# Performance work log

Measured on AMD Instinct MI355X. Metric: run time of the kernel, lower is better.

Reference implementation:

```python
import jax, jax.numpy as jnp
import numpy as np

B, N, D, H, COND = 1, 1024, 1024, 16, 128
S = 2 * N          # noisy tokens + clean x0 tokens
BS = 16            # diffusion block size
HD = D // H        # head dim = 64


def _ln(x, w):
    # LayerNorm module: F.layer_norm in fp32, then scale by weight (no bias)
    x = x.astype(jnp.float32)
    mu = jnp.mean(x, axis=-1, keepdims=True)
    var = jnp.var(x, axis=-1, keepdims=True)
    return (x - mu) / jnp.sqrt(var + 1e-5) * w


def _rotate_half(x):
    x1, x2 = jnp.split(x, 2, axis=-1)
    return jnp.concatenate([-x2, x1], axis=-1)


def _block_diff_mask(s, n, bs):
    q = jnp.arange(s)[:, None]
    k = jnp.arange(s)[None, :]
    fq = q >= n
    fk = k >= n
    bq = jnp.where(fq, (q - n) // bs, q // bs)
    bk = jnp.where(fk, (k - n) // bs, k // bs)
    diag = (bq == bk) & (fq == fk)
    off = (bq > bk) & fk & (~fq)
    caus = (bq >= bk) & fk & fq
    return diag | off | caus


def setup_inputs() -> dict:
    key = jax.random.key(0)
    ks = jax.random.split(key, 8)
    inv = 1.0 / (10000.0 ** (jnp.arange(0, HD, 2, dtype=jnp.float32) / HD))  # [32]
    t = jnp.arange(N, dtype=jnp.float32)[:, None] * inv[None, :]
    return {
        "x": jax.random.normal(ks[0], (B, S, D), jnp.float32),
        "c": jax.random.normal(ks[1], (B, COND), jnp.float32),
        "cos": jnp.cos(t),
        "sin": jnp.sin(t),
        "norm1_w": jnp.ones((D,), jnp.float32),
        "qkv_w": jax.random.normal(ks[2], (3 * D, D), jnp.float32) * (D ** -0.5),
        "attn_out_w": jax.random.normal(ks[3], (D, D), jnp.float32) * (D ** -0.5),
        "norm2_w": jnp.ones((D,), jnp.float32),
        "mlp_w1": jax.random.normal(ks[4], (4 * D, D), jnp.float32) * (D ** -0.5),
        "mlp_b1": jnp.zeros((4 * D,), jnp.float32),
        "mlp_w2": jax.random.normal(ks[5], (D, 4 * D), jnp.float32) * ((4 * D) ** -0.5),
        "mlp_b2": jnp.zeros((D,), jnp.float32),
        "adaLN_w": jax.random.normal(ks[6], (6 * D, COND), jnp.float32) * 0.02,
        "adaLN_b": jax.random.normal(ks[7], (6 * D,), jnp.float32) * 0.02,
    }


def reference(x, c, cos, sin, norm1_w, qkv_w, attn_out_w, norm2_w,
              mlp_w1, mlp_b1, mlp_w2, mlp_b2, adaLN_w, adaLN_b):
    # adaLN modulation: [B, 6D] -> six [B, 1, D] tensors
    mods = (c @ adaLN_w.T + adaLN_b)[:, None, :]
    sh_msa, sc_msa, g_msa, sh_mlp, sc_mlp, g_mlp = jnp.split(mods, 6, axis=-1)

    x_skip = x
    h = _ln(x, norm1_w) * (1 + sc_msa) + sh_msa  # modulate_fused

    # rotary tables broadcast to qkv rank 5 (torchscript path: applied to q, k AND v)
    cs = jnp.concatenate([cos, cos], axis=-1)[None, :, None, None, :]  # [1,N,1,1,HD]
    sn = jnp.concatenate([sin, sin], axis=-1)[None, :, None, None, :]

    def qkv_of(xh):  # xh: [B, N, D]
        qkv = (xh @ qkv_w.T).reshape(B, N, 3, H, HD)
        return qkv * cs + _rotate_half(qkv) * sn

    # halves processed separately (both use positions 0..N-1), then concatenated
    qkv = jnp.concatenate([qkv_of(h[:, :N]), qkv_of(h[:, N:])], axis=1)  # [B,S,3,H,HD]

    q = jnp.transpose(qkv[:, :, 0], (0, 2, 1, 3))  # [B,H,S,HD]
    k = jnp.transpose(qkv[:, :, 1], (0, 2, 1, 3))
    v = jnp.transpose(qkv[:, :, 2], (0, 2, 1, 3))

    scores = jnp.einsum('bhqd,bhkd->bhqk', q, k) / np.sqrt(HD).astype(np.float32)
    mask = _block_diff_mask(S, N, BS)  # [S,S] bool, block-diag | offset-causal | block-causal
    scores = jnp.where(mask[None, None], scores, -jnp.inf)
    attn = jax.nn.softmax(scores, axis=-1)
    o = jnp.einsum('bhqk,bhkd->bhqd', attn, v)
    o = jnp.transpose(o, (0, 2, 1, 3)).reshape(B, S, D)

    # inference bias_dropout_add_scale: gate * out + residual (dropout is identity)
    x2 = g_msa * (o @ attn_out_w.T) + x_skip
    h2 = _ln(x2, norm2_w) * (1 + sc_mlp) + sh_mlp
    m = jax.nn.gelu(h2 @ mlp_w1.T + mlp_b1, approximate=True) @ mlp_w2.T + mlp_b2
    return g_mlp * m + x2
```

## Files before the change

kernel.cpp:

```cpp
#include <hip/hip_runtime.h>
#include <math.h>

#define SS 2048
#define NN 1024
#define DD 1024
#define HH 16
#define CONDD 128

typedef unsigned short ushort;
typedef unsigned int uint;
typedef __bf16 bf16x8 __attribute__((ext_vector_type(8)));
typedef float f32x4 __attribute__((ext_vector_type(4)));
typedef short s16x4 __attribute__((ext_vector_type(4)));
typedef ushort u16x8 __attribute__((ext_vector_type(8)));

__device__ __forceinline__ float gelu_fast(float x) {
    float t = x + 0.044715f * x * x * x;
    float e = __builtin_exp2f(-2.3022081446f * t);
    return x * __builtin_amdgcn_rcpf(1.0f + e);
}

__device__ __forceinline__ ushort f2bf(float x) {
    uint u = __float_as_uint(x);
    u += 0x7fff + ((u >> 16) & 1);
    return (ushort)(u >> 16);
}

__device__ __forceinline__ float bf2f(ushort u) {
    return __uint_as_float(((uint)u) << 16);
}

__device__ __forceinline__ float ldf(const float* p) { return *p; }
__device__ __forceinline__ float ldf(const ushort* p) { return bf2f(*p); }

__device__ __forceinline__ void gload16(const ushort* g, ushort* l) {
    __builtin_amdgcn_global_load_lds(
        (const __attribute__((address_space(1))) void*)g,
        (__attribute__((address_space(3))) void*)l, 16, 0, 0);
}

template <int N>
__device__ __forceinline__ void wait_vm() {
    if constexpr (N == 0)      asm volatile("s_waitcnt vmcnt(0)" ::: "memory");
    else if constexpr (N == 2) asm volatile("s_waitcnt vmcnt(2)" ::: "memory");
    else if constexpr (N == 3) asm volatile("s_waitcnt vmcnt(3)" ::: "memory");
}

__device__ __forceinline__ f32x4 mfma16(s16x4 a, s16x4 b, f32x4 c) {
#if __has_builtin(__builtin_amdgcn_mfma_f32_16x16x16bf16_1k)
    return __builtin_amdgcn_mfma_f32_16x16x16bf16_1k(a, b, c, 0, 0, 0);
#else
    asm("v_mfma_f32_16x16x16_bf16 %0, %1, %2, %0" : "+v"(c) : "v"(a), "v"(b));
    return c;
#endif
}

__global__ void k_cast4(const float* __restrict__ s0, const float* __restrict__ s1,
                        const float* __restrict__ s2, const float* __restrict__ s3,
                        ushort* __restrict__ dst) {
    size_t gid = ((size_t)blockIdx.x * 256 + threadIdx.x) * 4;
    const float* src;
    size_t off;
    if (gid < (3ull << 20))      { src = s0; off = 0; }
    else if (gid < (4ull << 20)) { src = s1; off = 3ull << 20; }
    else if (gid < (8ull << 20)) { src = s2; off = 4ull << 20; }
    else                         { src = s3; off = 8ull << 20; }
    float4 v = *(const float4*)(src + (gid - off));
    ushort4 o = {f2bf(v.x), f2bf(v.y), f2bf(v.z), f2bf(v.w)};
    *(ushort4*)(dst + gid) = o;
}

__global__ void k_adaln(const float* __restrict__ c, const float* __restrict__ w,
                        const float* __restrict__ b, float* __restrict__ mods) {
    int o = blockIdx.x * 256 + threadIdx.x;
    float s = b[o];
    const float* wr = w + (size_t)o * CONDD;
    for (int k = 0; k < CONDD; ++k) s += c[k] * wr[k];
    mods[o] = s;
}

template <typename IT>
__global__ void k_ln_mod(const IT* __restrict__ x, const float* __restrict__ w,
                         const float* __restrict__ mods, int sh_idx, int sc_idx,
                         ushort* __restrict__ out) {
    int row = blockIdx.x;
    int tid = threadIdx.x;
    const IT* xr = x + (size_t)row * DD;
    float lx[4];
    float s = 0.f, s2 = 0.f;
    for (int i = 0; i < 4; ++i) {
        float v = ldf(&xr[tid + i * 256]);
        lx[i] = v; s += v; s2 += v * v;
    }
    __shared__ float rs[256], rs2[256];
    rs[tid] = s; rs2[tid] = s2; __syncthreads();
    for (int off = 128; off > 0; off >>= 1) {
        if (tid < off) { rs[tid] += rs[tid + off]; rs2[tid] += rs2[tid + off]; }
        __syncthreads();
    }
    float mu = rs[0] * (1.0f / DD);
    float var = rs2[0] * (1.0f / DD) - mu * mu;
    float rstd = rsqrtf(var + 1e-5f);
    const float* sh = mods + sh_idx * DD;
    const float* sc = mods + sc_idx * DD;
    ushort* orow = out + (size_t)row * DD;
    for (int i = 0; i < 4; ++i) {
        int d = tid + i * 256;
        orow[d] = f2bf((lx[i] - mu) * rstd * w[d] * (1.0f + sc[d]) + sh[d]);
    }
}

template <int TM, int TN, int MODE, typename OT>
__global__ __launch_bounds__(512) void k_gemm_mfma(
        const ushort* __restrict__ A, const ushort* __restrict__ W,
        const float* __restrict__ bias, const float* __restrict__ gate,
        const void* __restrict__ resid, OT* __restrict__ C,
        int M, int Nout, int K) {
    constexpr int WTM = TM / 2, WTN = TN / 4;
    constexpr int FM = WTM / 16, FN = WTN / 16;
    constexpr int BUFE = (TM + TN) * 64;
    constexpr int NA = TM / 64, NB = TN / 64;
    constexpr int LPW = NA + NB;
    __shared__ ushort lds[3 * BUFE];

    int tid = threadIdx.x;
    int lane = tid & 63, wave = tid >> 6;
    int wr = wave >> 2, wc = wave & 3;
    int l15 = lane & 15, l4 = lane >> 4;

    int orig = blockIdx.y * gridDim.x + blockIdx.x;
    int xcd = orig & 7;
    int idx = orig >> 3;
    int Nx = gridDim.x >> 3;
    int grp = 8 * Nx;
    int sm = idx / grp;
    int r = idx % grp;
    int ng = r >> 3;
    int mi2 = r & 7;
    int m0 = (sm * 8 + mi2) * TM;
    int n0 = (xcd * Nx + ng) * TN;

    f32x4 acc[FM][FN] = {};

    const ushort* pA[NA];
    const ushort* pB[NB];
    int dA[NA], dB[NB];
#pragma unroll
    for (int i = 0; i < NA; ++i) {
        int cb = (wave * NA + i) * 64;
        int ch = cb + lane;
        int row = ch >> 3;
        int kc = (ch & 7) ^ (row & 7);
        pA[i] = A + (size_t)(m0 + row) * K + kc * 8;
        dA[i] = cb * 8;
    }
#pragma unroll
    for (int i = 0; i < NB; ++i) {
        int cb = (wave * NB + i) * 64;
        int ch = cb + lane;
        int row = ch >> 3;
        int kc = (ch & 7) ^ (row & 7);
        pB[i] = W + (size_t)(n0 + row) * K + kc * 8;
        dB[i] = TM * 64 + cb * 8;
    }
    int offA[2][FM], offB[2][FN];
#pragma unroll
    for (int sub = 0; sub < 2; ++sub) {
#pragma unroll
        for (int mi = 0; mi < FM; ++mi) {
            int row = wr * WTM + mi * 16 + l15;
            int pos = ((sub << 2) | l4) ^ (row & 7);
            offA[sub][mi] = row * 64 + pos * 8;
        }
#pragma unroll
        for (int ni = 0; ni < FN; ++ni) {
            int row = wc * WTN + ni * 16 + l15;
            int pos = ((sub << 2) | l4) ^ (row & 7);
            offB[sub][ni] = TM * 64 + row * 64 + pos * 8;
        }
    }

    auto stage = [&](int buf) {
        ushort* base = lds + buf * BUFE;
#pragma unroll
        for (int i = 0; i < NA; ++i) { gload16(pA[i], base + dA[i]); pA[i] += 64; }
#pragma unroll
        for (int i = 0; i < NB; ++i) { gload16(pB[i], base + dB[i]); pB[i] += 64; }
    };

    auto compute = [&](int buf) {
        const ushort* base = lds + buf * BUFE;
#pragma unroll
        for (int sub = 0; sub < 2; ++sub) {
            bf16x8 af[FM], bw[FN];
#pragma unroll
            for (int mi = 0; mi < FM; ++mi)
                af[mi] = *(const bf16x8*)&base[offA[sub][mi]];
#pragma unroll
            for (int ni = 0; ni < FN; ++ni)
                bw[ni] = *(const bf16x8*)&base[offB[sub][ni]];
#pragma unroll
            for (int mi = 0; mi < FM; ++mi)
#pragma unroll
                for (int ni = 0; ni < FN; ++ni)
                    acc[mi][ni] = __builtin_amdgcn_mfma_f32_16x16x32_bf16(
                        af[mi], bw[ni], acc[mi][ni], 0, 0, 0);
        }
    };

    int nk = K >> 6;
    auto iter = [&](int t, int bufc, int bufs) {
        if (t + 1 < nk) wait_vm<LPW>(); else wait_vm<0>();
        __builtin_amdgcn_s_barrier();
        __builtin_amdgcn_sched_barrier(0);
        if (t + 2 < nk) stage(bufs);
        compute(bufc);
    };

    stage(0);
    stage(1);
    for (int t = 0; t < nk; t += 3) {
        iter(t, 0, 2);
        if (t + 1 < nk) iter(t + 1, 1, 0);
        if (t + 2 < nk) iter(t + 2, 2, 1);
    }

    const float*  rf = (const float*)resid;
    const ushort* rb = (const ushort*)resid;
#pragma unroll
    for (int mi = 0; mi < FM; ++mi) {
#pragma unroll
        for (int r2 = 0; r2 < 4; ++r2) {
            int m = m0 + wr * WTM + mi * 16 + l4 * 4 + r2;
#pragma unroll
            for (int ni = 0; ni < FN; ++ni) {
                int n = n0 + wc * WTN + ni * 16 + l15;
                float v = acc[mi][ni][r2];
                if (MODE == 1) v = gate[n] * v + rf[(size_t)m * Nout + n];
                if (MODE == 2) v = gelu_fast(v + bias[n]);
                if (MODE == 3) v = gate[n] * (v + bias[n]) + bf2f(rb[(size_t)m * Nout + n]);
                if (sizeof(OT) == 2) C[(size_t)m * Nout + n] = (OT)f2bf(v);
                else                 C[(size_t)m * Nout + n] = (OT)v;
            }
        }
    }
}

__global__ void k_rope2(const ushort* __restrict__ qkvb, const float* __restrict__ cosT,
                        const float* __restrict__ sinT, ushort* __restrict__ qb,
                        ushort* __restrict__ kb, ushort* __restrict__ vT) {
    __shared__ ushort vt[64][65];
    int h = blockIdx.x & 15;
    int st = blockIdx.x >> 4;
    int s0 = st * 64;
    int tid = threadIdx.x;
#pragma unroll
    for (int i = 0; i < 8; ++i) {
        int idx = tid + i * 256;
        int sl = idx >> 5, j = idx & 31;
        int s = s0 + sl;
        int pos = s & (NN - 1);
        float cv = cosT[pos * 32 + j], sv = sinT[pos * 32 + j];
        const ushort* row = qkvb + (size_t)s * 3072 + h * 64;
        float x1 = bf2f(row[j]), x2 = bf2f(row[j + 32]);
        qb[(size_t)s * DD + h * 64 + j]      = f2bf((x1 * cv - x2 * sv) * 0.18033688011f);
        qb[(size_t)s * DD + h * 64 + j + 32] = f2bf((x2 * cv + x1 * sv) * 0.18033688011f);
        x1 = bf2f(row[1024 + j]); x2 = bf2f(row[1024 + j + 32]);
        kb[(size_t)s * DD + h * 64 + j]      = f2bf(x1 * cv - x2 * sv);
        kb[(size_t)s * DD + h * 64 + j + 32] = f2bf(x2 * cv + x1 * sv);
        x1 = bf2f(row[2048 + j]); x2 = bf2f(row[2048 + j + 32]);
        vt[sl][j]      = f2bf(x1 * cv - x2 * sv);
        vt[sl][j + 32] = f2bf(x2 * cv + x1 * sv);
    }
    __syncthreads();
    int drow = tid >> 2, sc = (tid & 3) * 16;
    u16x8 a, b;
#pragma unroll
    for (int i = 0; i < 8; ++i) { a[i] = vt[sc + i][drow]; b[i] = vt[sc + 8 + i][drow]; }
    size_t base = (size_t)(h * 64 + drow) * SS + s0 + sc;
    *(u16x8*)&vT[base] = a;
    *(u16x8*)&vT[base + 8] = b;
}

struct KVTile { bf16x8 k0, k1; s16x4 v0, v1, v2, v3; };

__global__ __launch_bounds__(256) void k_attn4(
        const ushort* __restrict__ qb, const ushort* __restrict__ kb,
        const ushort* __restrict__ vT, ushort* __restrict__ o) {
    __shared__ float Ml[2][4][16], Ll[2][4][16];
    __shared__ float Ob[2][4][16][68];

    int id = blockIdx.x;
    int h = id & 15;
    int bq = 63 - (id >> 4);
    int tid = threadIdx.x;
    int wave = tid >> 6;
    int lane = tid & 63;
    int l15 = lane & 15, l4 = lane >> 4;
    int hb = h * 64;

    const int q0A = bq * 16, q0B = NN + bq * 16;
    bf16x8 qA0 = *(const bf16x8*)&qb[(size_t)(q0A + l15) * DD + hb + l4 * 8];
    bf16x8 qA1 = *(const bf16x8*)&qb[(size_t)(q0A + l15) * DD + hb + 32 + l4 * 8];
    bf16x8 qB0 = *(const bf16x8*)&qb[(size_t)(q0B + l15) * DD + hb + l4 * 8];
    bf16x8 qB1 = *(const bf16x8*)&qb[(size_t)(q0B + l15) * DD + hb + 32 + l4 * 8];

    float mA = -1e30f, lA = 0.f, mB = -1e30f, lB = 0.f;
    f32x4 oA0 = {}, oA1 = {}, oA2 = {}, oA3 = {};
    f32x4 oB0 = {}, oB1 = {}, oB2 = {}, oB3 = {};

    auto loadT = [&](int kbase) {
        KVTile t;
        const ushort* kr = kb + (size_t)(kbase + l15) * DD + hb + l4 * 8;
        t.k0 = *(const bf16x8*)kr;
        t.k1 = *(const bf16x8*)(kr + 32);
        const ushort* vr = vT + (size_t)(hb + l15) * SS + kbase + l4 * 4;
        t.v0 = *(const s16x4*)vr;
        t.v1 = *(const s16x4*)(vr + 16 * SS);
        t.v2 = *(const s16x4*)(vr + 32 * SS);
        t.v3 = *(const s16x4*)(vr + 48 * SS);
        return t;
    };

    auto step = [&](const KVTile& t, bf16x8 Q0, bf16x8 Q1, float& m, float& l,
                    f32x4& O0, f32x4& O1, f32x4& O2, f32x4& O3) {
        f32x4 s = {};
        s = __builtin_amdgcn_mfma_f32_16x16x32_bf16(t.k0, Q0, s, 0, 0, 0);
        s = __builtin_amdgcn_mfma_f32_16x16x32_bf16(t.k1, Q1, s, 0, 0, 0);
        float tm = fmaxf(fmaxf(s[0], s[1]), fmaxf(s[2], s[3]));
        tm = fmaxf(tm, __shfl_xor(tm, 16));
        tm = fmaxf(tm, __shfl_xor(tm, 32));
        if (!__all(tm <= m + 8.0f)) {
            float mn = fmaxf(m, tm);
            float alpha = exp2f(m - mn);
            l *= alpha;
            O0 *= alpha; O1 *= alpha; O2 *= alpha; O3 *= alpha;
            m = mn;
        }
        float p0 = exp2f(s[0] - m), p1 = exp2f(s[1] - m);
        float p2 = exp2f(s[2] - m), p3 = exp2f(s[3] - m);
        float rsum = (p0 + p1) + (p2 + p3);
        rsum += __shfl_xor(rsum, 16);
        rsum += __shfl_xor(rsum, 32);
        l += rsum;
        s16x4 pf;
        pf[0] = (short)f2bf(p0); pf[1] = (short)f2bf(p1);
        pf[2] = (short)f2bf(p2); pf[3] = (short)f2bf(p3);
        O0 = mfma16(t.v0, pf, O0);
        O1 = mfma16(t.v1, pf, O1);
        O2 = mfma16(t.v2, pf, O2);
        O3 = mfma16(t.v3, pf, O3);
    };

    if (wave == 0) {
        KVTile td = loadT(q0A);
        step(td, qA0, qA1, mA, lA, oA0, oA1, oA2, oA3);
    }
    KVTile cur, nxt;
    if (wave <= bq) cur = loadT(NN + wave * 16);
    for (int t = wave; t <= bq; t += 4) {
        int tn = t + 4;
        if (tn <= bq) nxt = loadT(NN + tn * 16);
        if (t < bq) step(cur, qA0, qA1, mA, lA, oA0, oA1, oA2, oA3);
        step(cur, qB0, qB1, mB, lB, oB0, oB1, oB2, oB3);
        cur = nxt;
    }

    if (l4 == 0) {
        Ml[0][wave][l15] = mA; Ll[0][wave][l15] = lA;
        Ml[1][wave][l15] = mB; Ll[1][wave][l15] = lB;
    }
    *(f32x4*)&Ob[0][wave][l15][l4 * 4]      = oA0;
    *(f32x4*)&Ob[0][wave][l15][l4 * 4 + 16] = oA1;
    *(f32x4*)&Ob[0][wave][l15][l4 * 4 + 32] = oA2;
    *(f32x4*)&Ob[0][wave][l15][l4 * 4 + 48] = oA3;
    *(f32x4*)&Ob[1][wave][l15][l4 * 4]      = oB0;
    *(f32x4*)&Ob[1][wave][l15][l4 * 4 + 16] = oB1;
    *(f32x4*)&Ob[1][wave][l15][l4 * 4 + 32] = oB2;
    *(f32x4*)&Ob[1][wave][l15][l4 * 4 + 48] = oB3;
    __syncthreads();

    int s = tid >> 7;
    int qr = (tid >> 3) & 15;
    int db = (tid & 7) * 8;
    float m0 = Ml[s][0][qr], m1 = Ml[s][1][qr], m2 = Ml[s][2][qr], m3 = Ml[s][3][qr];
    float ms = fmaxf(fmaxf(m0, m1), fmaxf(m2, m3));
    float a0 = exp2f(m0 - ms), a1 = exp2f(m1 - ms);
    float a2 = exp2f(m2 - ms), a3 = exp2f(m3 - ms);
    float lt = a0 * Ll[s][0][qr] + a1 * Ll[s][1][qr] + a2 * Ll[s][2][qr] + a3 * Ll[s][3][qr];
    float inv = 1.0f / lt;
    int q0s = (s == 0) ? q0A : q0B;
    u16x8 outv;
#pragma unroll
    for (int j = 0; j < 8; ++j) {
        float v = a0 * Ob[s][0][qr][db + j] + a1 * Ob[s][1][qr][db + j] +
                  a2 * Ob[s][2][qr][db + j] + a3 * Ob[s][3][qr][db + j];
        outv[j] = f2bf(v * inv);
    }
    *(u16x8*)&o[(size_t)(q0s + qr) * DD + hb + db] = outv;
}

extern "C" void kernel_launch(void* const* d_in, const int* in_sizes, int n_in,
                              void* d_out, int out_size, void* d_ws, size_t ws_size,
                              hipStream_t stream) {
    const float* x          = (const float*)d_in[0];
    const float* c          = (const float*)d_in[1];
    const float* cosT       = (const float*)d_in[2];
    const float* sinT       = (const float*)d_in[3];
    const float* norm1_w    = (const float*)d_in[4];
    const float* qkv_w      = (const float*)d_in[5];
    const float* attn_out_w = (const float*)d_in[6];
    const float* norm2_w    = (const float*)d_in[7];
    const float* mlp_w1     = (const float*)d_in[8];
    const float* mlp_b1     = (const float*)d_in[9];
    const float* mlp_w2     = (const float*)d_in[10];
    const float* mlp_b2     = (const float*)d_in[11];
    const float* adaLN_w    = (const float*)d_in[12];
    const float* adaLN_b    = (const float*)d_in[13];
    float* out = (float*)d_out;

    char* p = (char*)d_ws;
    float*  mods = (float*)p;   p += 6 * DD * 4;
    ushort* qkvb = (ushort*)p;  p += (size_t)SS * 3 * DD * 2;
    ushort* qb   = (ushort*)p;  p += (size_t)SS * DD * 2;
    ushort* kb   = (ushort*)p;  p += (size_t)SS * DD * 2;
    ushort* vT   = (ushort*)p;  p += (size_t)SS * DD * 2;
    ushort* x2b  = (ushort*)p;  p += (size_t)SS * DD * 2;
    ushort* hbuf = (ushort*)p;  p += (size_t)SS * DD * 2;
    ushort* obuf = (ushort*)p;  p += (size_t)SS * DD * 2;
    ushort* wq   = (ushort*)p;  p += (size_t)3 * DD * DD * 2;
    ushort* wo   = (ushort*)p;  p += (size_t)DD * DD * 2;
    ushort* w1   = (ushort*)p;  p += (size_t)4 * DD * DD * 2;
    ushort* w2   = (ushort*)p;  p += (size_t)4 * DD * DD * 2;
    ushort* m1   = qkvb;

    k_cast4<<<(12 << 20) / 1024, 256, 0, stream>>>(qkv_w, attn_out_w, mlp_w1, mlp_w2, wq);

    k_adaln<<<6 * DD / 256, 256, 0, stream>>>(c, adaLN_w, adaLN_b, mods);
    k_ln_mod<float><<<SS, 256, 0, stream>>>(x, norm1_w, mods, 0, 1, hbuf);

    dim3 g1(3 * DD / 128, SS / 64);
    k_gemm_mfma<64, 128, 0, ushort><<<g1, 512, 0, stream>>>(
        hbuf, wq, nullptr, nullptr, nullptr, qkvb, SS, 3 * DD, DD);
    k_rope2<<<512, 256, 0, stream>>>(qkvb, cosT, sinT, qb, kb, vT);
    k_attn4<<<HH * 64, 256, 0, stream>>>(qb, kb, vT, obuf);

    dim3 g2(DD / 64, SS / 64);
    k_gemm_mfma<64, 64, 1, ushort><<<g2, 512, 0, stream>>>(
        obuf, wo, nullptr, mods + 2 * DD, x, x2b, SS, DD, DD);
    k_ln_mod<ushort><<<SS, 256, 0, stream>>>(x2b, norm2_w, mods, 3, 4, hbuf);

    dim3 g3(4 * DD / 128, SS / 64);
    k_gemm_mfma<64, 128, 2, ushort><<<g3, 512, 0, stream>>>(
        hbuf, w1, mlp_b1, nullptr, nullptr, m1, SS, 4 * DD, DD);
    dim3 g4(DD / 64, SS / 64);
    k_gemm_mfma<64, 64, 3, float><<<g4, 512, 0, stream>>>(
        m1, w2, mlp_b2, mods + 5 * DD, x2b, out, SS, DD, 4 * DD);
}
```

Baseline: 147.2 us.

## Load GEMM weight fragments directly into registers, staging only A through LDS

The MFMA GEMM no longer stages the weight (B) tile through LDS. Each wave now loads its B fragments straight from global memory into a three-slot register ring, one k-step ahead, while A keeps the triple-buffered global_load_lds path. The aim is to cut LDS footprint, LDS read traffic and staging instructions, which may also allow more blocks per CU. In exchange, B is fetched with strided, less coalesced per-lane 16-byte loads, the two wave rows duplicate the same B loads, and register pressure rises.

After: 271.2 us. +84.3%, slower.

```diff
diff --git a/kernel.cpp b/kernel.cpp
--- a/kernel.cpp
+++ b/kernel.cpp
@@ -42,6 +42,7 @@
 template <int N>
 __device__ __forceinline__ void wait_vm() {
     if constexpr (N == 0)      asm volatile("s_waitcnt vmcnt(0)" ::: "memory");
+    else if constexpr (N == 1) asm volatile("s_waitcnt vmcnt(1)" ::: "memory");
     else if constexpr (N == 2) asm volatile("s_waitcnt vmcnt(2)" ::: "memory");
     else if constexpr (N == 3) asm volatile("s_waitcnt vmcnt(3)" ::: "memory");
 }
@@ -118,9 +119,9 @@
         int M, int Nout, int K) {
     constexpr int WTM = TM / 2, WTN = TN / 4;
     constexpr int FM = WTM / 16, FN = WTN / 16;
-    constexpr int BUFE = (TM + TN) * 64;
-    constexpr int NA = TM / 64, NB = TN / 64;
-    constexpr int LPW = NA + NB;
+    constexpr int BUFE = TM * 64;
+    constexpr int NA = TM / 64;
+    constexpr int NBR = FN * 2;
     __shared__ ushort lds[3 * BUFE];
 
     int tid = threadIdx.x;
@@ -143,8 +144,7 @@
     f32x4 acc[FM][FN] = {};
 
     const ushort* pA[NA];
-    const ushort* pB[NB];
-    int dA[NA], dB[NB];
+    int dA[NA];
 #pragma unroll
     for (int i = 0; i < NA; ++i) {
         int cb = (wave * NA + i) * 64;
@@ -154,75 +154,69 @@
         pA[i] = A + (size_t)(m0 + row) * K + kc * 8;
         dA[i] = cb * 8;
     }
-#pragma unroll
-    for (int i = 0; i < NB; ++i) {
-        int cb = (wave * NB + i) * 64;
-        int ch = cb + lane;
-        int row = ch >> 3;
-        int kc = (ch & 7) ^ (row & 7);
-        pB[i] = W + (size_t)(n0 + row) * K + kc * 8;
-        dB[i] = TM * 64 + cb * 8;
-    }
-    int offA[2][FM], offB[2][FN];
-#pragma unroll
-    for (int sub = 0; sub < 2; ++sub) {
+    const ushort* pB[NBR];
+#pragma unroll
+    for (int sub = 0; sub < 2; ++sub)
+#pragma unroll
+        for (int ni = 0; ni < FN; ++ni) {
+            int row = n0 + wc * WTN + ni * 16 + l15;
+            int ch = (sub << 2) | l4;
+            pB[sub * FN + ni] = W + (size_t)row * K + ch * 8;
+        }
+    int offA[2][FM];
+#pragma unroll
+    for (int sub = 0; sub < 2; ++sub)
 #pragma unroll
         for (int mi = 0; mi < FM; ++mi) {
             int row = wr * WTM + mi * 16 + l15;
             int pos = ((sub << 2) | l4) ^ (row & 7);
             offA[sub][mi] = row * 64 + pos * 8;
         }
-#pragma unroll
-        for (int ni = 0; ni < FN; ++ni) {
-            int row = wc * WTN + ni * 16 + l15;
-            int pos = ((sub << 2) | l4) ^ (row & 7);
-            offB[sub][ni] = TM * 64 + row * 64 + pos * 8;
-        }
-    }
-
-    auto stage = [&](int buf) {
+
+    bf16x8 b0[NBR], b1[NBR], b2[NBR];
+
+    auto stageA = [&](int buf) {
         ushort* base = lds + buf * BUFE;
 #pragma unroll
         for (int i = 0; i < NA; ++i) { gload16(pA[i], base + dA[i]); pA[i] += 64; }
-#pragma unroll
-        for (int i = 0; i < NB; ++i) { gload16(pB[i], base + dB[i]); pB[i] += 64; }
-    };
-
-    auto compute = [&](int buf) {
+    };
+    auto loadB = [&](bf16x8* slot) {
+#pragma unroll
+        for (int i = 0; i < NBR; ++i) { slot[i] = *(const bf16x8*)pB[i]; pB[i] += 64; }
+    };
+    auto compute = [&](int buf, const bf16x8* bs) {
         const ushort* base = lds + buf * BUFE;
 #pragma unroll
         for (int sub = 0; sub < 2; ++sub) {
-            bf16x8 af[FM], bw[FN];
+            bf16x8 af[FM];
 #pragma unroll
             for (int mi = 0; mi < FM; ++mi)
                 af[mi] = *(const bf16x8*)&base[offA[sub][mi]];
 #pragma unroll
-            for (int ni = 0; ni < FN; ++ni)
-                bw[ni] = *(const bf16x8*)&base[offB[sub][ni]];
-#pragma unroll
             for (int mi = 0; mi < FM; ++mi)
 #pragma unroll
                 for (int ni = 0; ni < FN; ++ni)
                     acc[mi][ni] = __builtin_amdgcn_mfma_f32_16x16x32_bf16(
-                        af[mi], bw[ni], acc[mi][ni], 0, 0, 0);
+                        af[mi], bs[sub * FN + ni], acc[mi][ni], 0, 0, 0);
         }
     };
 
     int nk = K >> 6;
-    auto iter = [&](int t, int bufc, int bufs) {
-        if (t + 1 < nk) wait_vm<LPW>(); else wait_vm<0>();
+    stageA(0);
+    loadB(b0);
+    stageA(1);
+    auto iter = [&](int t, int bufc, int bufs, bf16x8* buse, bf16x8* bload) {
+        if (t + 1 < nk) wait_vm<NA>(); else wait_vm<0>();
         __builtin_amdgcn_s_barrier();
         __builtin_amdgcn_sched_barrier(0);
-        if (t + 2 < nk) stage(bufs);
-        compute(bufc);
-    };
-
-    stage(0);
-    stage(1);
+        if (t + 1 < nk) loadB(bload);
+        if (t + 2 < nk) stageA(bufs);
+        compute(bufc, buse);
+    };
     for (int t = 0; t < nk; t += 3) {
-        iter(t, 0, 2);
-        if (t + 1 < nk) iter(t + 1, 1, 0);
-        if (t + 2 < nk) iter(t + 2, 2, 1);
+        iter(t, 0, 2, b0, b1);
+        if (t + 1 < nk) iter(t + 1, 1, 0, b1, b2);
+        if (t + 2 < nk) iter(t + 2, 2, 1, b2, b0);
     }
 
     const float*  rf = (const float*)resid;
```
